# Kernel optimization log

Measured on AMD Instinct MI355X. Metric: run time of the kernel, lower is better.

## Reference

```python
import jax, jax.numpy as jnp
import numpy as np
from jax import lax

# Faithful JAX translation of ConvAttention (enc=True, mask=False), the core
# kernel-headroom op of Conv_Transformer. Key observation: the per-(s,t)-pair
# conv2 over concat(Q[...,s], K[...,t]) is linear, so it decomposes exactly as
# conv(Q_s, W_q) + conv(K_t, W_k) + bias, where W_q/W_k are the first/second
# half of conv2's input channels. This reproduces the same math without
# materializing the [b, 2c, h, w, s, t] tensor or looping over time.

B, C, H, W, S = 4, 64, 64, 64, 20
K_SIZE = 3


def _conv_same(x, w):
    # x: [N, Cin, H, W], w: [Cout, Cin, kh, kw]
    return lax.conv_general_dilated(
        x, w, window_strides=(1, 1), padding='SAME',
        dimension_numbers=('NCHW', 'OIHW', 'NCHW'))


def setup_inputs() -> dict:
    key = jax.random.key(0)
    k1, k2, k3, k4, k5 = jax.random.split(key, 5)
    x = jax.random.normal(k1, (B, C, H, W, S), dtype=jnp.float32)
    w1 = jax.random.normal(k2, (3 * C, C, 1, 1), dtype=jnp.float32) * 0.05
    b1 = jax.random.normal(k3, (3 * C,), dtype=jnp.float32) * 0.05
    w2 = jax.random.normal(k4, (1, 2 * C, K_SIZE, K_SIZE), dtype=jnp.float32) * 0.05
    b2 = jax.random.normal(k5, (1,), dtype=jnp.float32) * 0.05
    return {'x': x, 'w1': w1, 'b1': b1, 'w2': w2, 'b2': b2}


def reference(x, w1, b1, w2, b2):
    b, c, h, w, s = x.shape
    # conv1 (1x1) per timestep -> QKV: [b, 3c, h, w, s]
    qkv = jnp.einsum('bchws,oc->bohws', x, w1[:, :, 0, 0]) \
        + b1[None, :, None, None, None]
    Q, K, V = jnp.split(qkv, 3, axis=1)  # each [b, c, h, w, s]

    # Decompose conv2 over concatenated channels.
    Wq, Wk = w2[:, :c], w2[:, c:]  # each [1, c, kh, kw]

    def per_time_conv(t5, wgt):
        # t5: [b, c, h, w, s] -> scores [b, h, w, s]
        flat = jnp.moveaxis(t5, -1, 1).reshape(b * s, c, h, w)
        out = _conv_same(flat, wgt)  # [b*s, 1, h, w]
        return out.reshape(b, s, h, w).transpose(0, 2, 3, 1)

    A = per_time_conv(Q, Wq)  # [b, h, w, s]  (query index)
    Bk = per_time_conv(K, Wk)  # [b, h, w, t]  (key index)

    # score[b,h,w,t,s] = conv2(concat(Q_s, K_t)) ; softmax over t (keys)
    scores = A[:, :, :, None, :] + Bk[:, :, :, :, None] + b2[0]
    attn = jax.nn.softmax(scores, axis=-2)  # [b, h, w, t, s]

    # V_out[b,c,h,w,s] = sum_t attn[...,t,s] * V[...,t]
    V_out = jnp.einsum('bhwts,bchwt->bchws', attn, V)
    return V_out
```

## Files before the change

kernel.cpp:

```cpp
#include <hip/hip_runtime.h>
#include <math.h>

#define Bb 4
#define Cc 64
#define Hh 64
#define Ww 64
#define Ss 20

constexpr int XC = Hh * Ww * Ss;
constexpr int XH = Ww * Ss;
constexpr int XW = Ss;
constexpr int XB = Cc * XC;
constexpr int NSITE = Bb * Hh * Ww;
constexpr int PSMF  = NSITE * Ss;


__global__ void ct_fold_weights(const float* __restrict__ w1,
                                const float* __restrict__ b1,
                                const float* __restrict__ w2,
                                float* __restrict__ ws) {
    int tid = threadIdx.x;
    if (tid < 576) {
        int tap = tid >> 6, cp = tid & 63;
        float acc = 0.f;
        #pragma unroll 8
        for (int c = 0; c < 64; ++c)
            acc += w2[(64 + c) * 9 + tap] * w1[(64 + c) * 64 + cp];
        ws[tid] = acc;
    } else if (tid < 585) {
        int tap = tid - 576;
        float acc = 0.f;
        for (int c = 0; c < 64; ++c)
            acc += w2[(64 + c) * 9 + tap] * b1[64 + c];
        ws[576 + tap] = acc;
    }
}

__global__ __launch_bounds__(640) void ct_conv_sm(
        const float* __restrict__ x,
        const float* __restrict__ ws,
        float* __restrict__ psm) {
    __shared__ float weff[576];
    __shared__ float btL[9];
    __shared__ float bkp[4][32][20];
    __shared__ float psmL[32][20];
    int tid = threadIdx.x;

    for (int i = tid; i < 576; i += 640) weff[i] = ws[i];
    if (tid < 9) btL[tid] = ws[576 + tid];

    int g = (blockIdx.x & 7) * 64 + (blockIdx.x >> 3);
    int wh = g & 1;
    int h  = (g >> 1) & 63;
    int b  = g >> 7;

    int cg = tid / 160, r = tid % 160;
    int w16 = r / 5, t4 = r % 5;
    int w = wh * 32 + w16;

    float vmask[9];
    int off[9];
    #pragma unroll
    for (int dh = 0; dh < 3; ++dh) {
        int hh = h + dh - 1;
        float hv = (hh >= 0 && hh < Hh) ? 1.f : 0.f;
        int hcl = hh < 0 ? 0 : (hh > Hh - 1 ? Hh - 1 : hh);
        #pragma unroll
        for (int dw = 0; dw < 3; ++dw) {
            int wc = w + dw - 1;
            float wvd = (wc >= 0 && wc < Ww) ? 1.f : 0.f;
            int wcl = wc < 0 ? 0 : (wc > Ww - 1 ? Ww - 1 : wc);
            vmask[dh * 3 + dw] = hv * wvd;
            off[dh * 3 + dw] = hcl * XH + wcl * XW;
        }
    }
    __syncthreads();

    float4 acc = make_float4(0.f, 0.f, 0.f, 0.f);
    const float* xb = x + b * XB + cg * 16 * XC + t4 * 4;
    #pragma unroll 2
    for (int c = 0; c < 16; ++c) {
        const float* xc = xb + c * XC;
        #pragma unroll
        for (int tap = 0; tap < 9; ++tap) {
            float wv = weff[tap * 64 + cg * 16 + c] * vmask[tap];
            const float4 xv = *reinterpret_cast<const float4*>(xc + off[tap]);
            acc.x = fmaf(wv, xv.x, acc.x);
            acc.y = fmaf(wv, xv.y, acc.y);
            acc.z = fmaf(wv, xv.z, acc.z);
            acc.w = fmaf(wv, xv.w, acc.w);
        }
    }
    *reinterpret_cast<float4*>(&bkp[cg][w16][t4 * 4]) = acc;
    __syncthreads();

    {
        int sw = tid / 20, t = tid % 20;
        float v = bkp[0][sw][t] + bkp[1][sw][t] + bkp[2][sw][t] + bkp[3][sw][t];
        int wsit = wh * 32 + sw;
        float bs = 0.f;
        #pragma unroll
        for (int dh = 0; dh < 3; ++dh) {
            int hh = h + dh - 1;
            if (hh < 0 || hh >= Hh) continue;
            #pragma unroll
            for (int dw = 0; dw < 3; ++dw) {
                int wc = wsit + dw - 1;
                if (wc < 0 || wc >= Ww) continue;
                bs += btL[dh * 3 + dw];
            }
        }
        psmL[sw][t] = v + bs;
    }
    __syncthreads();

    if (tid < 32) {
        float p[20];
        #pragma unroll
        for (int i = 0; i < 20; ++i) p[i] = psmL[tid][i];
        float m = p[0];
        #pragma unroll
        for (int i = 1; i < 20; ++i) m = fmaxf(m, p[i]);
        float ssum = 0.f;
        #pragma unroll
        for (int i = 0; i < 20; ++i) { p[i] = __expf(p[i] - m); ssum += p[i]; }
        float inv = 1.f / ssum;
        #pragma unroll
        for (int i = 0; i < 20; ++i) psmL[tid][i] = p[i] * inv;
    }
    __syncthreads();

    {
        int sw = tid / 20, t = tid % 20;
        int site = b * 4096 + h * 64 + wh * 32 + sw;
        psm[site * 20 + t] = psmL[sw][t];
    }
}

__global__ __launch_bounds__(256) void ct_attn_lite(
        const float* __restrict__ x,
        const float* __restrict__ w1,
        const float* __restrict__ b1,
        const float* __restrict__ psm,
        float* __restrict__ out) {
    __shared__ float w1t[64 * 65];
    __shared__ float psmL[8][20];
    __shared__ float xsh[8][65];
    int tid = threadIdx.x;
    #pragma unroll
    for (int k = 0; k < 16; ++k) {
        int j = tid + k * 256;
        int r = j >> 6, q = j & 63;
        w1t[q * 65 + r] = w1[8192 + j];
    }

    int site0 = blockIdx.x * 8;
    if (tid < 160) {
        int si = tid / 20, i = tid % 20;
        psmL[si][i] = psm[(site0 + si) * 20 + i];
    }
    __syncthreads();

    int si = tid & 7, cg = tid >> 3;
    int site = site0 + si;
    int b = site >> 12, hw = site & 4095;

    #pragma unroll
    for (int k = 0; k < 2; ++k) {
        int c = cg * 2 + k;
        const float* xp = x + (b * 64 + c) * XC + hw * 20;
        float xbv = 0.f;
        #pragma unroll
        for (int i = 0; i < 5; ++i) {
            float4 xv = reinterpret_cast<const float4*>(xp)[i];
            xbv = fmaf(psmL[si][4 * i],     xv.x, xbv);
            xbv = fmaf(psmL[si][4 * i + 1], xv.y, xbv);
            xbv = fmaf(psmL[si][4 * i + 2], xv.z, xbv);
            xbv = fmaf(psmL[si][4 * i + 3], xv.w, xbv);
        }
        xsh[si][c] = xbv;
    }
    __syncthreads();

    #pragma unroll
    for (int k = 0; k < 2; ++k) {
        int c = cg * 2 + k;
        float R = b1[128 + c];
        #pragma unroll 8
        for (int cp = 0; cp < 64; ++cp)
            R = fmaf(w1t[cp * 65 + c], xsh[si][cp], R);
        float* op = out + (b * 64 + c) * XC + hw * 20;
        float4 rv = make_float4(R, R, R, R);
        #pragma unroll
        for (int s4 = 0; s4 < 5; ++s4)
            reinterpret_cast<float4*>(op)[s4] = rv;
    }
}

extern "C" void kernel_launch(void* const* d_in, const int* in_sizes, int n_in,
                              void* d_out, int out_size, void* d_ws, size_t ws_size,
                              hipStream_t stream) {
    const float* x  = (const float*)d_in[0];
    const float* w1 = (const float*)d_in[1];
    const float* b1 = (const float*)d_in[2];
    const float* w2 = (const float*)d_in[3];
    float* ws  = (float*)d_ws;
    float* psm = ws + 640;
    float* out = (float*)d_out;

    ct_fold_weights<<<1, 640, 0, stream>>>(w1, b1, w2, ws);
    ct_conv_sm<<<512, 640, 0, stream>>>(x, ws, psm);
    ct_attn_lite<<<2048, 256, 0, stream>>>(x, w1, b1, psm, out);
}
```

Before: 74.28 us.

## Halve conv block width and software-pipeline channel loads with register double buffering

The conv+softmax kernel now has each block cover 16 w-positions instead of 32, running 1024 blocks of 320 threads with a launch-bounds occupancy hint. The channel loop is software-pipelined: the nine tap float4 values for the next two channels are prefetched into two register buffers while the current ones are consumed. This aims to hide global load latency and improve occupancy, at the cost of more registers per thread and duplicate halo loads across smaller blocks.

```diff
diff --git a/kernel.cpp b/kernel.cpp
--- a/kernel.cpp
+++ b/kernel.cpp
@@ -36,27 +36,27 @@
     }
 }
 
-__global__ __launch_bounds__(640) void ct_conv_sm(
+__global__ __launch_bounds__(320, 5) void ct_conv_sm(
         const float* __restrict__ x,
         const float* __restrict__ ws,
         float* __restrict__ psm) {
     __shared__ float weff[576];
     __shared__ float btL[9];
-    __shared__ float bkp[4][32][20];
-    __shared__ float psmL[32][20];
+    __shared__ float bkp[4][16][20];
+    __shared__ float psmL[16][20];
     int tid = threadIdx.x;
 
-    for (int i = tid; i < 576; i += 640) weff[i] = ws[i];
+    for (int i = tid; i < 576; i += 320) weff[i] = ws[i];
     if (tid < 9) btL[tid] = ws[576 + tid];
 
-    int g = (blockIdx.x & 7) * 64 + (blockIdx.x >> 3);
-    int wh = g & 1;
-    int h  = (g >> 1) & 63;
-    int b  = g >> 7;
-
-    int cg = tid / 160, r = tid % 160;
+    int g = (blockIdx.x & 7) * 128 + (blockIdx.x >> 3);
+    int wq = g & 3;
+    int h  = (g >> 2) & 63;
+    int b  = g >> 8;
+
+    int cg = tid / 80, r = tid % 80;
     int w16 = r / 5, t4 = r % 5;
-    int w = wh * 32 + w16;
+    int w = wq * 16 + w16;
 
     float vmask[9];
     int off[9];
@@ -76,28 +76,55 @@
     }
     __syncthreads();
 
+    const float* xb = x + b * XB + cg * 16 * XC + t4 * 4;
     float4 acc = make_float4(0.f, 0.f, 0.f, 0.f);
-    const float* xb = x + b * XB + cg * 16 * XC + t4 * 4;
-    #pragma unroll 2
-    for (int c = 0; c < 16; ++c) {
-        const float* xc = xb + c * XC;
+    float4 pvA[9], pvB[9];
+    #pragma unroll
+    for (int tap = 0; tap < 9; ++tap)
+        pvA[tap] = *reinterpret_cast<const float4*>(xb + off[tap]);
+    #pragma unroll
+    for (int tap = 0; tap < 9; ++tap)
+        pvB[tap] = *reinterpret_cast<const float4*>(xb + XC + off[tap]);
+
+    #pragma unroll 1
+    for (int c = 0; c < 16; c += 2) {
+        const float* xn2 = xb + (c + 2 < 16 ? c + 2 : c) * XC;
+        const float* xn3 = xb + (c + 3 < 16 ? c + 3 : c + 1) * XC;
+
         #pragma unroll
         for (int tap = 0; tap < 9; ++tap) {
             float wv = weff[tap * 64 + cg * 16 + c] * vmask[tap];
-            const float4 xv = *reinterpret_cast<const float4*>(xc + off[tap]);
-            acc.x = fmaf(wv, xv.x, acc.x);
-            acc.y = fmaf(wv, xv.y, acc.y);
-            acc.z = fmaf(wv, xv.z, acc.z);
-            acc.w = fmaf(wv, xv.w, acc.w);
-        }
-    }
+            float4 v = pvA[tap];
+            acc.x = fmaf(wv, v.x, acc.x);
+            acc.y = fmaf(wv, v.y, acc.y);
+            acc.z = fmaf(wv, v.z, acc.z);
+            acc.w = fmaf(wv, v.w, acc.w);
+        }
+        #pragma unroll
+        for (int tap = 0; tap < 9; ++tap)
+            pvA[tap] = *reinterpret_cast<const float4*>(xn2 + off[tap]);
+
+        #pragma unroll
+        for (int tap = 0; tap < 9; ++tap) {
+            float wv = weff[tap * 64 + cg * 16 + c + 1] * vmask[tap];
+            float4 v = pvB[tap];
+            acc.x = fmaf(wv, v.x, acc.x);
+            acc.y = fmaf(wv, v.y, acc.y);
+            acc.z = fmaf(wv, v.z, acc.z);
+            acc.w = fmaf(wv, v.w, acc.w);
+        }
+        #pragma unroll
+        for (int tap = 0; tap < 9; ++tap)
+            pvB[tap] = *reinterpret_cast<const float4*>(xn3 + off[tap]);
+    }
+
     *reinterpret_cast<float4*>(&bkp[cg][w16][t4 * 4]) = acc;
     __syncthreads();
 
     {
         int sw = tid / 20, t = tid % 20;
         float v = bkp[0][sw][t] + bkp[1][sw][t] + bkp[2][sw][t] + bkp[3][sw][t];
-        int wsit = wh * 32 + sw;
+        int wsit = wq * 16 + sw;
         float bs = 0.f;
         #pragma unroll
         for (int dh = 0; dh < 3; ++dh) {
@@ -114,7 +141,7 @@
     }
     __syncthreads();
 
-    if (tid < 32) {
+    if (tid < 16) {
         float p[20];
         #pragma unroll
         for (int i = 0; i < 20; ++i) p[i] = psmL[tid][i];
@@ -132,8 +159,8 @@
 
     {
         int sw = tid / 20, t = tid % 20;
-        int site = b * 4096 + h * 64 + wh * 32 + sw;
-        psm[site * 20 + t] = psmL[sw][t];
+        int base = (b * 4096 + h * 64 + wq * 16) * 20;
+        psm[base + tid] = psmL[sw][t];
     }
 }
 
@@ -209,6 +236,6 @@
     float* out = (float*)d_out;
 
     ct_fold_weights<<<1, 640, 0, stream>>>(w1, b1, w2, ws);
-    ct_conv_sm<<<512, 640, 0, stream>>>(x, ws, psm);
+    ct_conv_sm<<<1024, 320, 0, stream>>>(x, ws, psm);
     ct_attn_lite<<<2048, 256, 0, stream>>>(x, w1, b1, psm, out);
 }
```

After: 77.76 us. +4.7%, slower.
